# Kernel optimization log

Hardware: AMD Instinct MI355X
Metric: run time of the kernel (lower is better)

## Reference

```python
import jax, jax.numpy as jnp
from jax import lax
import numpy as np

GROUPS = 32

def setup_inputs() -> dict:
    key = jax.random.key(0)
    ks = jax.random.split(key, 12)
    B, C, H, O, N = 4, 256, 256, 256, 4096
    s = 0.02  # small init scale to keep logits in a stable range
    x  = jax.random.normal(ks[0], (B, C, N), dtype=jnp.float32)
    Wk = jax.random.normal(ks[1], (H, C), dtype=jnp.float32) * s
    bk = jax.random.normal(ks[2], (H,), dtype=jnp.float32) * s
    Wq = jax.random.normal(ks[3], (H, C), dtype=jnp.float32) * s
    bq = jax.random.normal(ks[4], (H,), dtype=jnp.float32) * s
    W1 = jax.random.normal(ks[5], (H, C), dtype=jnp.float32) * s
    b1 = jax.random.normal(ks[6], (H,), dtype=jnp.float32) * s
    # grouped conv1d kernel: (out_ch, in_ch // groups, kw) in 'OIH' layout
    W2 = jax.random.normal(ks[7], (H, H // GROUPS, 3), dtype=jnp.float32) * s
    b2 = jax.random.normal(ks[8], (H,), dtype=jnp.float32) * s
    W3 = jax.random.normal(ks[9], (O, H), dtype=jnp.float32) * s
    b3 = jax.random.normal(ks[10], (O,), dtype=jnp.float32) * s
    return {"x": x, "Wk": Wk, "bk": bk, "Wq": Wq, "bq": bq,
            "W1": W1, "b1": b1, "W2": W2, "b2": b2, "W3": W3, "b3": b3}


def reference(x, Wk, bk, Wq, bq, W1, b1, W2, b2, W3, b3):
    # k: 1x1 conv then permute(0,2,1) -> [B, N, H]
    k = jnp.einsum('hc,bcn->bnh', Wk, x) + bk
    # q: 1x1 conv -> [B, H, N]
    q = jnp.einsum('hc,bcn->bhn', Wq, x) + bq[None, :, None]
    # sim = softmax(k @ q, dim=-2): softmax over the FIRST N axis (rows)
    sim = jax.nn.softmax(jnp.einsum('bnh,bhm->bnm', k, q), axis=-2)  # [B, N, N]
    # v path: 1x1 conv -> grouped 3-tap conv (pad=1) -> ReLU -> 1x1 conv
    v1 = jnp.einsum('hc,bcn->bhn', W1, x) + b1[None, :, None]
    v2 = lax.conv_general_dilated(
        v1, W2, window_strides=(1,), padding='SAME',
        feature_group_count=GROUPS,
        dimension_numbers=('NCH', 'OIH', 'NCH')) + b2[None, :, None]
    v2 = jax.nn.relu(v2)
    v = jnp.einsum('oh,bhn->bon', W3, v2) + b3[None, :, None]  # [B, O, N]
    # out = v @ sim -> [B, O, N]
    return jnp.einsum('bon,bnm->bom', v, sim)
```

## Files before the change

kernel.cpp:

```cpp
#include <hip/hip_runtime.h>


#define B_ 4
#define C_ 256
#define H_ 256
#define O_ 256
#define N_ 4096
#define NSPLIT 4
#define SPAN (N_ / NSPLIT)
#define ITERS (SPAN / 32)

typedef short short8 __attribute__((ext_vector_type(8)));
typedef float floatx4 __attribute__((ext_vector_type(4)));
typedef float floatx16 __attribute__((ext_vector_type(16)));

__device__ __forceinline__ unsigned short f2bf(float f) {
  unsigned u = __float_as_uint(f);
  u = (u + 0x7fffu + ((u >> 16) & 1u)) >> 16;
  return (unsigned short)u;
}
__device__ __forceinline__ float bf2f(unsigned short u) {
  return __uint_as_float(((unsigned)u) << 16);
}
__device__ __forceinline__ floatx4 mfma16(short8 a, short8 b, floatx4 c) {
  return __builtin_amdgcn_mfma_f32_16x16x32_bf16(a, b, c, 0, 0, 0);
}
__device__ __forceinline__ floatx16 mfma32(short8 a, short8 b, floatx16 c) {
  return __builtin_amdgcn_mfma_f32_32x32x16_bf16(a, b, c, 0, 0, 0);
}

__global__ __launch_bounds__(256) void prep_kernel(
    const float* __restrict__ Wk, const float* __restrict__ Wq,
    const float* __restrict__ W1, const float* __restrict__ W3,
    unsigned short* __restrict__ wk, unsigned short* __restrict__ wq,
    unsigned short* __restrict__ w1, unsigned short* __restrict__ w3) {
  int i = blockIdx.x * 256 + threadIdx.x;
  wk[i] = f2bf(Wk[i]);
  wq[i] = f2bf(Wq[i]);
  w1[i] = f2bf(W1[i]);
  w3[i] = f2bf(W3[i]);
}

__global__ __launch_bounds__(256) void transpose_kernel(
    const float* __restrict__ x, unsigned short* __restrict__ xt) {
  __shared__ unsigned short tile[64][66];
  const int gid = blockIdx.x;
  const int b  = gid >> 8;
  const int ct = (gid >> 6) & 3;
  const int nt = gid & 63;
  const int c0 = ct * 64, n0 = nt * 64;
  const int t = threadIdx.x;
  const float* xb = x + ((size_t)b * C_ + c0) * N_ + n0;
#pragma unroll
  for (int rr = 0; rr < 4; ++rr) {
    const int c = (t >> 4) + rr * 16;
    const floatx4 v = *reinterpret_cast<const floatx4*>(
        xb + (size_t)c * N_ + (t & 15) * 4);
#pragma unroll
    for (int i = 0; i < 4; ++i) tile[c][(t & 15) * 4 + i] = f2bf(v[i]);
  }
  __syncthreads();
  unsigned short* xo = xt + ((size_t)b * N_ + n0) * C_ + c0;
#pragma unroll
  for (int rr = 0; rr < 2; ++rr) {
    const int nr = (t >> 3) + rr * 32;
    short8 pk;
#pragma unroll
    for (int i = 0; i < 8; ++i) pk[i] = (short)tile[(t & 7) * 8 + i][nr];
    *reinterpret_cast<short8*>(xo + (size_t)nr * C_ + (t & 7) * 8) = pk;
  }
}

__global__ __launch_bounds__(256) void gemm1_kernel(
    const unsigned short* __restrict__ xt,
    const unsigned short* __restrict__ wk, const unsigned short* __restrict__ wq,
    const unsigned short* __restrict__ w1,
    const float* __restrict__ bk, const float* __restrict__ bq,
    const float* __restrict__ b1,
    unsigned short* __restrict__ ko, unsigned short* __restrict__ qo,
    unsigned short* __restrict__ v1o) {
  const int lane = threadIdx.x & 63;
  const int wid  = blockIdx.x * 4 + (threadIdx.x >> 6);
  const int b  = wid >> 9;
  const int r  = wid & 511;
  const int nt = r >> 1;
  const int hh = r & 1;
  const int n0 = nt * 16;
  const int m  = lane & 15;
  const int q  = lane >> 4;

  const unsigned short* xrow = xt + ((size_t)(b * N_) + n0 + m) * C_;
  const unsigned short* Ws[3] = {wk, wq, w1};

  floatx4 acc[3][8];
  const floatx4 z = {0.f, 0.f, 0.f, 0.f};
#pragma unroll
  for (int o = 0; o < 3; ++o)
#pragma unroll
    for (int tt = 0; tt < 8; ++tt) acc[o][tt] = z;

  for (int cs = 0; cs < 8; ++cs) {
    const int cb = cs * 32 + q * 8;
    short8 af = *reinterpret_cast<const short8*>(xrow + cb);
#pragma unroll
    for (int o = 0; o < 3; ++o) {
#pragma unroll
      for (int tt = 0; tt < 8; ++tt) {
        const int h0 = (hh * 8 + tt) * 16;
        short8 bf = *reinterpret_cast<const short8*>(Ws[o] + (h0 + m) * C_ + cb);
        acc[o][tt] = mfma16(af, bf, acc[o][tt]);
      }
    }
  }

#pragma unroll
  for (int tt = 0; tt < 8; ++tt) {
    const int hbase = (hh * 8 + tt) * 2 + (m >> 3);
    const float bias = bk[(hh * 8 + tt) * 16 + m];
#pragma unroll
    for (int r2 = 0; r2 < 4; ++r2) {
      const int n = n0 + q * 4 + r2;
      const int hbl = hbase ^ (n & 7);
      ko[(b * N_ + n) * H_ + hbl * 8 + (m & 7)] = f2bf(acc[0][tt][r2] + bias);
    }
  }
  const float* biases[2] = {bq, b1};
  unsigned short* outs[2] = {qo, v1o};
#pragma unroll
  for (int o = 0; o < 2; ++o) {
#pragma unroll
    for (int tt = 0; tt < 8; ++tt) {
      const int h0 = (hh * 8 + tt) * 16;
      const float bias = biases[o][h0 + m];
#pragma unroll
      for (int r2 = 0; r2 < 4; ++r2) {
        const int n = n0 + q * 4 + r2;
        outs[o][(b * N_ + n) * H_ + h0 + m] = f2bf(acc[o + 1][tt][r2] + bias);
      }
    }
  }
}

__global__ __launch_bounds__(256) void conv_kernel(
    const unsigned short* __restrict__ v1, const float* __restrict__ W2,
    const float* __restrict__ b2, unsigned short* __restrict__ v2) {
  const int h   = threadIdx.x;
  const int blk = blockIdx.x;
  const int b   = blk >> 7;
  const int n0  = (blk & 127) * 32;
  const int g8  = h & ~7;

  float w[24];
#pragma unroll
  for (int i = 0; i < 24; ++i) w[i] = W2[h * 24 + i];
  const float bias = b2[h];
  const unsigned short* vb = v1 + (size_t)b * (N_ * H_) + g8;
  unsigned short* vo = v2 + (size_t)b * (N_ * H_) + h;

  float fp[8], fc[8], fn[8];
  if (n0 == 0) {
#pragma unroll
    for (int i = 0; i < 8; ++i) fp[i] = 0.f;
  } else {
    short8 u = *reinterpret_cast<const short8*>(vb + (size_t)(n0 - 1) * H_);
#pragma unroll
    for (int i = 0; i < 8; ++i) fp[i] = bf2f((unsigned short)u[i]);
  }
  {
    short8 u = *reinterpret_cast<const short8*>(vb + (size_t)n0 * H_);
#pragma unroll
    for (int i = 0; i < 8; ++i) fc[i] = bf2f((unsigned short)u[i]);
  }
#pragma unroll 1
  for (int ns = 0; ns < 32; ++ns) {
    const int n = n0 + ns;
    if (n + 1 < N_) {
      short8 u = *reinterpret_cast<const short8*>(vb + (size_t)(n + 1) * H_);
#pragma unroll
      for (int i = 0; i < 8; ++i) fn[i] = bf2f((unsigned short)u[i]);
    } else {
#pragma unroll
      for (int i = 0; i < 8; ++i) fn[i] = 0.f;
    }
    float acc = bias;
#pragma unroll
    for (int i = 0; i < 8; ++i)
      acc += w[i * 3] * fp[i] + w[i * 3 + 1] * fc[i] + w[i * 3 + 2] * fn[i];
    vo[(size_t)n * H_] = f2bf(fmaxf(acc, 0.f));
#pragma unroll
    for (int i = 0; i < 8; ++i) { fp[i] = fc[i]; fc[i] = fn[i]; }
  }
}

__global__ __launch_bounds__(256) void gemm2_kernel(
    const unsigned short* __restrict__ v2, const unsigned short* __restrict__ w3,
    const float* __restrict__ b3, unsigned short* __restrict__ vo) {
  const int lane = threadIdx.x & 63;
  const int wid  = blockIdx.x * 4 + (threadIdx.x >> 6);
  const int b  = wid >> 9;
  const int r  = wid & 511;
  const int nt = r >> 1;
  const int oh = r & 1;
  const int n0 = nt * 16;
  const int m  = lane & 15;
  const int q  = lane >> 4;

  const unsigned short* vrow = v2 + (b * N_ + n0 + m) * H_;

  floatx4 acc[8];
  const floatx4 z = {0.f, 0.f, 0.f, 0.f};
#pragma unroll
  for (int tt = 0; tt < 8; ++tt) acc[tt] = z;

  for (int hs = 0; hs < 8; ++hs) {
    const int hb = hs * 32 + q * 8;
    short8 bf = *reinterpret_cast<const short8*>(vrow + hb);
#pragma unroll
    for (int tt = 0; tt < 8; ++tt) {
      const int o0 = (oh * 8 + tt) * 16;
      short8 af = *reinterpret_cast<const short8*>(w3 + (o0 + m) * H_ + hb);
      acc[tt] = mfma16(af, bf, acc[tt]);
    }
  }

  const int n  = n0 + m;
  const int n32 = n & ~31;
  const int nb  = (n >> 3) & 3;
  const int nlo = n & 7;
#pragma unroll
  for (int tt = 0; tt < 8; ++tt) {
    const int o0 = (oh * 8 + tt) * 16;
    const floatx4 bb = *reinterpret_cast<const floatx4*>(b3 + o0 + q * 4);
#pragma unroll
    for (int r2 = 0; r2 < 4; ++r2) {
      const int o = o0 + q * 4 + r2;
      const int nbp = nb ^ ((o >> 1) & 3);
      vo[(b * O_ + o) * N_ + n32 + nbp * 8 + nlo] = f2bf(acc[tt][r2] + bb[r2]);
    }
  }
}

__global__ __launch_bounds__(256, 2) void attn_kernel(
    const unsigned short* __restrict__ kbf, const unsigned short* __restrict__ qbf,
    const unsigned short* __restrict__ vbf,
    unsigned short* __restrict__ pacc, float* __restrict__ pml) {
  __shared__ __attribute__((aligned(16))) char smem[2][32768];

  const int ln  = threadIdx.x & 63;
  const int wv  = threadIdx.x >> 6;
  const int gid = blockIdx.x;
  const int t8  = gid & 7;
  const int b   = t8 >> 1;
  const int s   = (t8 & 1) * 2 + ((gid >> 3) & 1);
  const int mw  = (gid >> 4) * 4 + wv;
  const int m0  = mw * 32;
  const int m   = ln & 31;
  const int hl  = ln >> 5;
  const int nbase = s * SPAN;

  const unsigned short* kb2 = kbf + (size_t)b * (N_ * H_);
  const unsigned short* vb2 = vbf + (size_t)b * (O_ * N_);

  const unsigned short* qrow = qbf + ((size_t)(b * N_) + m0 + m) * H_;
  short8 qf[16];
#pragma unroll
  for (int ks = 0; ks < 16; ++ks)
    qf[ks] = *reinterpret_cast<const short8*>(qrow + ks * 16 + hl * 8);

  floatx16 acc[8];
#pragma unroll
  for (int ot = 0; ot < 8; ++ot)
#pragma unroll
    for (int r = 0; r < 16; ++r) acc[ot][r] = 0.f;
  float Lp = 0.f;

  auto stage = [&](int bfi, int nc) {
    const int n0 = nbase + nc * 32;
    const char* kg  = (const char*)kb2 + (size_t)n0 * (H_ * 2);
    const char* vgb = (const char*)vb2 + (size_t)n0 * 2;
    char* lk = &smem[bfi][0];
    char* lv = &smem[bfi][16384];
#pragma unroll
    for (int j = 0; j < 4; ++j) {
      const int ofs = j * 4096 + wv * 1024 + ln * 16;
      __builtin_amdgcn_global_load_lds(
          (const __attribute__((address_space(1))) void*)(kg + ofs),
          (__attribute__((address_space(3))) void*)(lk + ofs), 16, 0, 0);
      const int o = ofs >> 6;
      __builtin_amdgcn_global_load_lds(
          (const __attribute__((address_space(1))) void*)(vgb + (size_t)o * (N_ * 2) + (ofs & 63)),
          (__attribute__((address_space(3))) void*)(lv + ofs), 16, 0, 0);
    }
  };

  stage(0, 0);
  int bufi = 0;

#pragma unroll 1
  for (int nc = 0; nc < ITERS; ++nc) {
    __syncthreads();
    if (nc + 1 < ITERS) stage(bufi ^ 1, nc + 1);

    const char* sk = &smem[bufi][0];
    const char* sv = &smem[bufi][16384];

    floatx16 sacc;
#pragma unroll
    for (int r = 0; r < 16; ++r) sacc[r] = 0.f;
#pragma unroll
    for (int ks = 0; ks < 16; ++ks) {
      short8 kf = *reinterpret_cast<const short8*>(
          sk + m * 512 + (((ks * 2 + hl) ^ (m & 7)) << 4));
      sacc = mfma32(kf, qf[ks], sacc);
    }

    float pv[16];
#pragma unroll
    for (int r = 0; r < 16; ++r) { pv[r] = __expf(sacc[r]); Lp += pv[r]; }

    unsigned wpk[8];
#pragma unroll
    for (int r4 = 0; r4 < 4; ++r4) {
      wpk[r4]     = (unsigned)f2bf(pv[r4])      | ((unsigned)f2bf(pv[r4 + 4])  << 16);
      wpk[r4 + 4] = (unsigned)f2bf(pv[r4 + 8])  | ((unsigned)f2bf(pv[r4 + 12]) << 16);
    }

    short8 pf0, pf1;
#pragma unroll
    for (int j = 0; j < 8; ++j) {
      const int srcLane = m + ((j >> 2) << 5);
      const int u0 = __shfl((int)wpk[j & 3],       srcLane);
      const int u1 = __shfl((int)wpk[(j & 3) + 4], srcLane);
      pf0[j] = (short)(hl ? (u0 >> 16) : (u0 & 0xffff));
      pf1[j] = (short)(hl ? (u1 >> 16) : (u1 & 0xffff));
    }

#pragma unroll
    for (int ot = 0; ot < 8; ++ot) {
      const int o  = ot * 32 + m;
      const int sw = (o >> 1) & 3;
      short8 vf0 = *reinterpret_cast<const short8*>(
          sv + o * 64 + ((hl ^ sw) << 4));
      short8 vf1 = *reinterpret_cast<const short8*>(
          sv + o * 64 + (((2 + hl) ^ sw) << 4));
      acc[ot] = mfma32(vf0, pf0, acc[ot]);
      acc[ot] = mfma32(vf1, pf1, acc[ot]);
    }
    bufi ^= 1;
  }

  float Lv = Lp + __shfl_xor(Lp, 32);
  const float invL = 1.f / Lv;
  const int pwid = (b * 128 + mw) * NSPLIT + s;
  unsigned short* pa = pacc + (size_t)pwid * (O_ * 32);
#pragma unroll
  for (int ot = 0; ot < 8; ++ot)
#pragma unroll
    for (int r = 0; r < 16; ++r) {
      const int row = (r & 3) + ((r >> 2) << 3) + (hl << 2);
      pa[(ot * 32 + row) * 32 + m] = f2bf(acc[ot][r] * invL);
    }
  if (hl == 0) pml[pwid * 32 + m] = Lv;
}

__global__ __launch_bounds__(256) void combine_kernel(
    const unsigned short* __restrict__ pacc, const float* __restrict__ pml,
    float* __restrict__ out) {
  const int blk = blockIdx.x;
  const int b   = blk >> 7;
  const int mw  = blk & 127;
  const int o   = threadIdx.x;
  const int base = (b * 128 + mw) * NSPLIT;

  __shared__ float w[NSPLIT][32];
  if (threadIdx.x < 32) {
    const int c = threadIdx.x;
    float L[NSPLIT], sum = 0.f;
#pragma unroll
    for (int sp = 0; sp < NSPLIT; ++sp) {
      L[sp] = pml[(base + sp) * 32 + c];
      sum += L[sp];
    }
    const float inv = 1.f / sum;
#pragma unroll
    for (int sp = 0; sp < NSPLIT; ++sp) w[sp][c] = L[sp] * inv;
  }
  __syncthreads();

  float res[32];
#pragma unroll
  for (int c = 0; c < 32; ++c) res[c] = 0.f;
#pragma unroll
  for (int sp = 0; sp < NSPLIT; ++sp) {
    const unsigned short* pa =
        pacc + (size_t)(base + sp) * (O_ * 32) + o * 32;
#pragma unroll
    for (int c8 = 0; c8 < 4; ++c8) {
      short8 u = *reinterpret_cast<const short8*>(pa + c8 * 8);
#pragma unroll
      for (int i = 0; i < 8; ++i)
        res[c8 * 8 + i] =
            fmaf(w[sp][c8 * 8 + i], bf2f((unsigned short)u[i]), res[c8 * 8 + i]);
    }
  }
  float* ob = out + ((size_t)(b * O_ + o)) * N_ + mw * 32;
#pragma unroll
  for (int c4 = 0; c4 < 8; ++c4) {
    floatx4 v4 = {res[c4 * 4], res[c4 * 4 + 1], res[c4 * 4 + 2], res[c4 * 4 + 3]};
    *reinterpret_cast<floatx4*>(ob + c4 * 4) = v4;
  }
}

extern "C" void kernel_launch(void* const* d_in, const int* in_sizes, int n_in,
                              void* d_out, int out_size, void* d_ws, size_t ws_size,
                              hipStream_t stream) {
  const float* x  = (const float*)d_in[0];
  const float* Wk = (const float*)d_in[1];
  const float* bk = (const float*)d_in[2];
  const float* Wq = (const float*)d_in[3];
  const float* bq = (const float*)d_in[4];
  const float* W1 = (const float*)d_in[5];
  const float* b1 = (const float*)d_in[6];
  const float* W2 = (const float*)d_in[7];
  const float* b2 = (const float*)d_in[8];
  const float* W3 = (const float*)d_in[9];
  const float* b3 = (const float*)d_in[10];
  float* out = (float*)d_out;

  char* ws = (char*)d_ws;
  const size_t SZ = (size_t)B_ * N_ * H_ * sizeof(unsigned short);
  unsigned short* wkbf = (unsigned short*)(ws);
  unsigned short* wqbf = (unsigned short*)(ws + 131072);
  unsigned short* w1bf = (unsigned short*)(ws + 262144);
  unsigned short* w3bf = (unsigned short*)(ws + 393216);
  char* base = ws + 524288;
  unsigned short* kbf  = (unsigned short*)(base);
  unsigned short* qbf  = (unsigned short*)(base + SZ);
  unsigned short* vbf  = (unsigned short*)(base + 2 * SZ);
  unsigned short* xtbf = (unsigned short*)(base + 3 * SZ);
  unsigned short* v1bf = (unsigned short*)(base + 4 * SZ);
  unsigned short* v2bf = (unsigned short*)(base + 5 * SZ);
  unsigned short* pacc = (unsigned short*)(base + 3 * SZ);
  float*          pml  = (float*)(base + 7 * SZ);

  prep_kernel<<<256, 256, 0, stream>>>(Wk, Wq, W1, W3, wkbf, wqbf, w1bf, w3bf);
  transpose_kernel<<<1024, 256, 0, stream>>>(x, xtbf);
  gemm1_kernel<<<512, 256, 0, stream>>>(xtbf, wkbf, wqbf, w1bf, bk, bq, b1,
                                        kbf, qbf, v1bf);
  conv_kernel<<<512, 256, 0, stream>>>(v1bf, W2, b2, v2bf);
  gemm2_kernel<<<512, 256, 0, stream>>>(v2bf, w3bf, b3, vbf);
  attn_kernel<<<512, 256, 0, stream>>>(kbf, qbf, vbf, pacc, pml);
  combine_kernel<<<512, 256, 0, stream>>>(pacc, pml, out);
}
```

Baseline: 272.8 us.

## Fuse conv with second GEMM, pre-tile K/V layouts, widen attention tile

The grouped conv and the W3 projection now run in one kernel that keeps the ReLU output in LDS, so the v2 round trip through global memory is gone. K and V are written in contiguous 32-row chunks laid out for the attention kernel's MFMA fragments, which makes LDS reads linear and unswizzled. Each attention wave now handles 64 query columns instead of 32, so every K/V LDS fragment feeds two MFMAs; this doubles the accumulator count, drops occupancy to one block per CU and halves the grid. Bf16 packing uses a perm-based truncate-with-rounding helper, and the combine kernel is resized to the 64-wide tiles.

```diff
diff --git a/kernel.cpp b/kernel.cpp
--- a/kernel.cpp
+++ b/kernel.cpp
@@ -27,6 +27,10 @@
 }
 __device__ __forceinline__ floatx16 mfma32(short8 a, short8 b, floatx16 c) {
   return __builtin_amdgcn_mfma_f32_32x32x16_bf16(a, b, c, 0, 0, 0);
+}
+__device__ __forceinline__ unsigned pack2bf(float a, float b) {
+  return __builtin_amdgcn_perm(__float_as_uint(b) + 0x8000u,
+                               __float_as_uint(a) + 0x8000u, 0x07060302u);
 }
 
 __global__ __launch_bounds__(256) void prep_kernel(
@@ -115,13 +119,13 @@
 
 #pragma unroll
   for (int tt = 0; tt < 8; ++tt) {
-    const int hbase = (hh * 8 + tt) * 2 + (m >> 3);
-    const float bias = bk[(hh * 8 + tt) * 16 + m];
+    const int ks16 = hh * 8 + tt;
+    const float bias = bk[ks16 * 16 + m];
 #pragma unroll
     for (int r2 = 0; r2 < 4; ++r2) {
       const int n = n0 + q * 4 + r2;
-      const int hbl = hbase ^ (n & 7);
-      ko[(b * N_ + n) * H_ + hbl * 8 + (m & 7)] = f2bf(acc[0][tt][r2] + bias);
+      ko[((size_t)(b * 128 + (n >> 5))) * 8192 + ks16 * 512 + (n & 31) * 16 + m] =
+          f2bf(acc[0][tt][r2] + bias);
     }
   }
   const float* biases[2] = {bq, b1};
@@ -141,106 +145,98 @@
   }
 }
 
-__global__ __launch_bounds__(256) void conv_kernel(
+__global__ __launch_bounds__(256) void convgemm2_kernel(
     const unsigned short* __restrict__ v1, const float* __restrict__ W2,
-    const float* __restrict__ b2, unsigned short* __restrict__ v2) {
+    const float* __restrict__ b2, const unsigned short* __restrict__ w3,
+    const float* __restrict__ b3, unsigned short* __restrict__ vo) {
+  __shared__ unsigned short v2L[32][264];
+
   const int h   = threadIdx.x;
   const int blk = blockIdx.x;
   const int b   = blk >> 7;
-  const int n0  = (blk & 127) * 32;
+  const int nc  = blk & 127;
+  const int n0  = nc * 32;
   const int g8  = h & ~7;
 
-  float w[24];
-#pragma unroll
-  for (int i = 0; i < 24; ++i) w[i] = W2[h * 24 + i];
-  const float bias = b2[h];
-  const unsigned short* vb = v1 + (size_t)b * (N_ * H_) + g8;
-  unsigned short* vo = v2 + (size_t)b * (N_ * H_) + h;
-
-  float fp[8], fc[8], fn[8];
-  if (n0 == 0) {
-#pragma unroll
-    for (int i = 0; i < 8; ++i) fp[i] = 0.f;
-  } else {
-    short8 u = *reinterpret_cast<const short8*>(vb + (size_t)(n0 - 1) * H_);
-#pragma unroll
-    for (int i = 0; i < 8; ++i) fp[i] = bf2f((unsigned short)u[i]);
-  }
   {
-    short8 u = *reinterpret_cast<const short8*>(vb + (size_t)n0 * H_);
-#pragma unroll
-    for (int i = 0; i < 8; ++i) fc[i] = bf2f((unsigned short)u[i]);
-  }
+    float w[24];
+#pragma unroll
+    for (int i = 0; i < 24; ++i) w[i] = W2[h * 24 + i];
+    const float bias = b2[h];
+    const unsigned short* vb = v1 + (size_t)b * (N_ * H_) + g8;
+
+    float fp[8], fc[8], fn[8];
+    if (n0 == 0) {
+#pragma unroll
+      for (int i = 0; i < 8; ++i) fp[i] = 0.f;
+    } else {
+      short8 u = *reinterpret_cast<const short8*>(vb + (size_t)(n0 - 1) * H_);
+#pragma unroll
+      for (int i = 0; i < 8; ++i) fp[i] = bf2f((unsigned short)u[i]);
+    }
+    {
+      short8 u = *reinterpret_cast<const short8*>(vb + (size_t)n0 * H_);
+#pragma unroll
+      for (int i = 0; i < 8; ++i) fc[i] = bf2f((unsigned short)u[i]);
+    }
 #pragma unroll 1
-  for (int ns = 0; ns < 32; ++ns) {
-    const int n = n0 + ns;
-    if (n + 1 < N_) {
-      short8 u = *reinterpret_cast<const short8*>(vb + (size_t)(n + 1) * H_);
-#pragma unroll
-      for (int i = 0; i < 8; ++i) fn[i] = bf2f((unsigned short)u[i]);
-    } else {
-#pragma unroll
-      for (int i = 0; i < 8; ++i) fn[i] = 0.f;
-    }
-    float acc = bias;
-#pragma unroll
-    for (int i = 0; i < 8; ++i)
-      acc += w[i * 3] * fp[i] + w[i * 3 + 1] * fc[i] + w[i * 3 + 2] * fn[i];
-    vo[(size_t)n * H_] = f2bf(fmaxf(acc, 0.f));
-#pragma unroll
-    for (int i = 0; i < 8; ++i) { fp[i] = fc[i]; fc[i] = fn[i]; }
-  }
-}
-
-__global__ __launch_bounds__(256) void gemm2_kernel(
-    const unsigned short* __restrict__ v2, const unsigned short* __restrict__ w3,
-    const float* __restrict__ b3, unsigned short* __restrict__ vo) {
-  const int lane = threadIdx.x & 63;
-  const int wid  = blockIdx.x * 4 + (threadIdx.x >> 6);
-  const int b  = wid >> 9;
-  const int r  = wid & 511;
-  const int nt = r >> 1;
-  const int oh = r & 1;
-  const int n0 = nt * 16;
-  const int m  = lane & 15;
-  const int q  = lane >> 4;
-
-  const unsigned short* vrow = v2 + (b * N_ + n0 + m) * H_;
-
-  floatx4 acc[8];
-  const floatx4 z = {0.f, 0.f, 0.f, 0.f};
-#pragma unroll
-  for (int tt = 0; tt < 8; ++tt) acc[tt] = z;
-
-  for (int hs = 0; hs < 8; ++hs) {
-    const int hb = hs * 32 + q * 8;
-    short8 bf = *reinterpret_cast<const short8*>(vrow + hb);
-#pragma unroll
-    for (int tt = 0; tt < 8; ++tt) {
-      const int o0 = (oh * 8 + tt) * 16;
-      short8 af = *reinterpret_cast<const short8*>(w3 + (o0 + m) * H_ + hb);
-      acc[tt] = mfma16(af, bf, acc[tt]);
-    }
-  }
-
-  const int n  = n0 + m;
-  const int n32 = n & ~31;
-  const int nb  = (n >> 3) & 3;
-  const int nlo = n & 7;
-#pragma unroll
-  for (int tt = 0; tt < 8; ++tt) {
-    const int o0 = (oh * 8 + tt) * 16;
-    const floatx4 bb = *reinterpret_cast<const floatx4*>(b3 + o0 + q * 4);
-#pragma unroll
-    for (int r2 = 0; r2 < 4; ++r2) {
-      const int o = o0 + q * 4 + r2;
-      const int nbp = nb ^ ((o >> 1) & 3);
-      vo[(b * O_ + o) * N_ + n32 + nbp * 8 + nlo] = f2bf(acc[tt][r2] + bb[r2]);
-    }
-  }
-}
-
-__global__ __launch_bounds__(256, 2) void attn_kernel(
+    for (int ns = 0; ns < 32; ++ns) {
+      const int n = n0 + ns;
+      if (n + 1 < N_) {
+        short8 u = *reinterpret_cast<const short8*>(vb + (size_t)(n + 1) * H_);
+#pragma unroll
+        for (int i = 0; i < 8; ++i) fn[i] = bf2f((unsigned short)u[i]);
+      } else {
+#pragma unroll
+        for (int i = 0; i < 8; ++i) fn[i] = 0.f;
+      }
+      float a = bias;
+#pragma unroll
+      for (int i = 0; i < 8; ++i)
+        a += w[i * 3] * fp[i] + w[i * 3 + 1] * fc[i] + w[i * 3 + 2] * fn[i];
+      v2L[ns][h] = f2bf(fmaxf(a, 0.f));
+#pragma unroll
+      for (int i = 0; i < 8; ++i) { fp[i] = fc[i]; fc[i] = fn[i]; }
+    }
+  }
+  __syncthreads();
+
+  const int ln = threadIdx.x & 63;
+  const int wv = threadIdx.x >> 6;
+  const int m  = ln & 31;
+  const int hl = ln >> 5;
+
+  floatx16 acc2[2];
+#pragma unroll
+  for (int ot = 0; ot < 2; ++ot)
+#pragma unroll
+    for (int r = 0; r < 16; ++r) acc2[ot][r] = 0.f;
+
+#pragma unroll
+  for (int ks = 0; ks < 16; ++ks) {
+    short8 bfr = *reinterpret_cast<const short8*>(&v2L[m][ks * 16 + hl * 8]);
+#pragma unroll
+    for (int ot = 0; ot < 2; ++ot) {
+      const int o0 = wv * 64 + ot * 32;
+      short8 afr = *reinterpret_cast<const short8*>(
+          w3 + (o0 + m) * H_ + ks * 16 + hl * 8);
+      acc2[ot] = mfma32(afr, bfr, acc2[ot]);
+    }
+  }
+
+  const int kn  = (m >> 4) & 1;
+  const int nlo = m & 15;
+  unsigned short* vc = vo + ((size_t)(b * 128 + nc) * 2 + kn) * 4096 + nlo;
+#pragma unroll
+  for (int ot = 0; ot < 2; ++ot)
+#pragma unroll
+    for (int r = 0; r < 16; ++r) {
+      const int o = wv * 64 + ot * 32 + (r & 3) + 8 * (r >> 2) + 4 * hl;
+      vc[o * 16] = f2bf(acc2[ot][r] + b3[o]);
+    }
+}
+
+__global__ __launch_bounds__(256, 1) void attn_kernel(
     const unsigned short* __restrict__ kbf, const unsigned short* __restrict__ qbf,
     const unsigned short* __restrict__ vbf,
     unsigned short* __restrict__ pacc, float* __restrict__ pml) {
@@ -249,35 +245,36 @@
   const int ln  = threadIdx.x & 63;
   const int wv  = threadIdx.x >> 6;
   const int gid = blockIdx.x;
-  const int t8  = gid & 7;
-  const int b   = t8 >> 1;
-  const int s   = (t8 & 1) * 2 + ((gid >> 3) & 1);
-  const int mw  = (gid >> 4) * 4 + wv;
-  const int m0  = mw * 32;
+  const int b   = gid & 3;
+  const int s   = (gid >> 2) & 3;
+  const int mt256 = gid >> 4;
+  const int mt64  = mt256 * 4 + wv;
+  const int m0  = mt64 * 64;
   const int m   = ln & 31;
   const int hl  = ln >> 5;
-  const int nbase = s * SPAN;
-
-  const unsigned short* kb2 = kbf + (size_t)b * (N_ * H_);
-  const unsigned short* vb2 = vbf + (size_t)b * (O_ * N_);
-
-  const unsigned short* qrow = qbf + ((size_t)(b * N_) + m0 + m) * H_;
-  short8 qf[16];
-#pragma unroll
-  for (int ks = 0; ks < 16; ++ks)
-    qf[ks] = *reinterpret_cast<const short8*>(qrow + ks * 16 + hl * 8);
-
-  floatx16 acc[8];
-#pragma unroll
-  for (int ot = 0; ot < 8; ++ot)
-#pragma unroll
-    for (int r = 0; r < 16; ++r) acc[ot][r] = 0.f;
-  float Lp = 0.f;
+  const int lane_base = m * 32 + hl * 16;
+
+  short8 qf[2][16];
+#pragma unroll
+  for (int mh = 0; mh < 2; ++mh) {
+    const unsigned short* qrow =
+        qbf + ((size_t)b * N_ + m0 + mh * 32 + m) * H_ + hl * 8;
+#pragma unroll
+    for (int ks = 0; ks < 16; ++ks)
+      qf[mh][ks] = *reinterpret_cast<const short8*>(qrow + ks * 16);
+  }
+
+  floatx16 acc[16];
+#pragma unroll
+  for (int t = 0; t < 16; ++t)
+#pragma unroll
+    for (int r = 0; r < 16; ++r) acc[t][r] = 0.f;
+  float Lp0 = 0.f, Lp1 = 0.f;
 
   auto stage = [&](int bfi, int nc) {
-    const int n0 = nbase + nc * 32;
-    const char* kg  = (const char*)kb2 + (size_t)n0 * (H_ * 2);
-    const char* vgb = (const char*)vb2 + (size_t)n0 * 2;
+    const size_t row = (size_t)(b * 128 + s * 32 + nc);
+    const char* kg = (const char*)(kbf + row * 8192);
+    const char* vg = (const char*)(vbf + row * 8192);
     char* lk = &smem[bfi][0];
     char* lv = &smem[bfi][16384];
 #pragma unroll
@@ -286,15 +283,15 @@
       __builtin_amdgcn_global_load_lds(
           (const __attribute__((address_space(1))) void*)(kg + ofs),
           (__attribute__((address_space(3))) void*)(lk + ofs), 16, 0, 0);
-      const int o = ofs >> 6;
       __builtin_amdgcn_global_load_lds(
-          (const __attribute__((address_space(1))) void*)(vgb + (size_t)o * (N_ * 2) + (ofs & 63)),
+          (const __attribute__((address_space(1))) void*)(vg + ofs),
           (__attribute__((address_space(3))) void*)(lv + ofs), 16, 0, 0);
     }
   };
 
   stage(0, 0);
   int bufi = 0;
+  const int hlsh = hl * 16;
 
 #pragma unroll 1
   for (int nc = 0; nc < ITERS; ++nc) {
@@ -304,81 +301,95 @@
     const char* sk = &smem[bufi][0];
     const char* sv = &smem[bufi][16384];
 
-    floatx16 sacc;
-#pragma unroll
-    for (int r = 0; r < 16; ++r) sacc[r] = 0.f;
+    floatx16 s0, s1;
+#pragma unroll
+    for (int r = 0; r < 16; ++r) { s0[r] = 0.f; s1[r] = 0.f; }
 #pragma unroll
     for (int ks = 0; ks < 16; ++ks) {
-      short8 kf = *reinterpret_cast<const short8*>(
-          sk + m * 512 + (((ks * 2 + hl) ^ (m & 7)) << 4));
-      sacc = mfma32(kf, qf[ks], sacc);
-    }
-
-    float pv[16];
-#pragma unroll
-    for (int r = 0; r < 16; ++r) { pv[r] = __expf(sacc[r]); Lp += pv[r]; }
-
-    unsigned wpk[8];
+      short8 kf = *reinterpret_cast<const short8*>(sk + lane_base + ks * 1024);
+      s0 = mfma32(kf, qf[0][ks], s0);
+      s1 = mfma32(kf, qf[1][ks], s1);
+    }
+
+    unsigned wpk0[8], wpk1[8];
 #pragma unroll
     for (int r4 = 0; r4 < 4; ++r4) {
-      wpk[r4]     = (unsigned)f2bf(pv[r4])      | ((unsigned)f2bf(pv[r4 + 4])  << 16);
-      wpk[r4 + 4] = (unsigned)f2bf(pv[r4 + 8])  | ((unsigned)f2bf(pv[r4 + 12]) << 16);
-    }
-
-    short8 pf0, pf1;
+      float a0 = __expf(s0[r4]),      b0 = __expf(s0[r4 + 4]);
+      float c0 = __expf(s0[r4 + 8]),  d0 = __expf(s0[r4 + 12]);
+      float a1 = __expf(s1[r4]),      b1 = __expf(s1[r4 + 4]);
+      float c1 = __expf(s1[r4 + 8]),  d1 = __expf(s1[r4 + 12]);
+      Lp0 += (a0 + b0) + (c0 + d0);
+      Lp1 += (a1 + b1) + (c1 + d1);
+      wpk0[r4]     = pack2bf(a0, b0);
+      wpk0[r4 + 4] = pack2bf(c0, d0);
+      wpk1[r4]     = pack2bf(a1, b1);
+      wpk1[r4 + 4] = pack2bf(c1, d1);
+    }
+
+    short8 pf[2][2];
 #pragma unroll
     for (int j = 0; j < 8; ++j) {
       const int srcLane = m + ((j >> 2) << 5);
-      const int u0 = __shfl((int)wpk[j & 3],       srcLane);
-      const int u1 = __shfl((int)wpk[(j & 3) + 4], srcLane);
-      pf0[j] = (short)(hl ? (u0 >> 16) : (u0 & 0xffff));
-      pf1[j] = (short)(hl ? (u1 >> 16) : (u1 & 0xffff));
+      const int u00 = __shfl((int)wpk0[j & 3],       srcLane);
+      const int u01 = __shfl((int)wpk0[(j & 3) + 4], srcLane);
+      const int u10 = __shfl((int)wpk1[j & 3],       srcLane);
+      const int u11 = __shfl((int)wpk1[(j & 3) + 4], srcLane);
+      pf[0][0][j] = (short)((unsigned)u00 >> hlsh);
+      pf[0][1][j] = (short)((unsigned)u01 >> hlsh);
+      pf[1][0][j] = (short)((unsigned)u10 >> hlsh);
+      pf[1][1][j] = (short)((unsigned)u11 >> hlsh);
     }
 
 #pragma unroll
     for (int ot = 0; ot < 8; ++ot) {
-      const int o  = ot * 32 + m;
-      const int sw = (o >> 1) & 3;
-      short8 vf0 = *reinterpret_cast<const short8*>(
-          sv + o * 64 + ((hl ^ sw) << 4));
-      short8 vf1 = *reinterpret_cast<const short8*>(
-          sv + o * 64 + (((2 + hl) ^ sw) << 4));
-      acc[ot] = mfma32(vf0, pf0, acc[ot]);
-      acc[ot] = mfma32(vf1, pf1, acc[ot]);
+#pragma unroll
+      for (int kn = 0; kn < 2; ++kn) {
+        short8 vf = *reinterpret_cast<const short8*>(
+            sv + lane_base + kn * 8192 + ot * 1024);
+        acc[ot]     = mfma32(vf, pf[0][kn], acc[ot]);
+        acc[8 + ot] = mfma32(vf, pf[1][kn], acc[8 + ot]);
+      }
     }
     bufi ^= 1;
   }
 
-  float Lv = Lp + __shfl_xor(Lp, 32);
-  const float invL = 1.f / Lv;
-  const int pwid = (b * 128 + mw) * NSPLIT + s;
-  unsigned short* pa = pacc + (size_t)pwid * (O_ * 32);
-#pragma unroll
-  for (int ot = 0; ot < 8; ++ot)
-#pragma unroll
-    for (int r = 0; r < 16; ++r) {
-      const int row = (r & 3) + ((r >> 2) << 3) + (hl << 2);
-      pa[(ot * 32 + row) * 32 + m] = f2bf(acc[ot][r] * invL);
-    }
-  if (hl == 0) pml[pwid * 32 + m] = Lv;
+  float Lv0 = Lp0 + __shfl_xor(Lp0, 32);
+  float Lv1 = Lp1 + __shfl_xor(Lp1, 32);
+  const float i0 = 1.f / Lv0, i1 = 1.f / Lv1;
+
+  const int pwid = (b * 64 + mt64) * NSPLIT + s;
+  unsigned short* pa = pacc + (size_t)pwid * (O_ * 64);
+#pragma unroll
+  for (int mh = 0; mh < 2; ++mh) {
+    const float inv = mh ? i1 : i0;
+#pragma unroll
+    for (int ot = 0; ot < 8; ++ot)
+#pragma unroll
+      for (int r = 0; r < 16; ++r) {
+        const int o = ot * 32 + (r & 3) + 8 * (r >> 2) + 4 * hl;
+        pa[o * 64 + mh * 32 + m] = f2bf(acc[mh * 8 + ot][r] * inv);
+      }
+  }
+  if (hl == 0) pml[pwid * 64 + m] = Lv0;
+  else         pml[pwid * 64 + 32 + m] = Lv1;
 }
 
 __global__ __launch_bounds__(256) void combine_kernel(
     const unsigned short* __restrict__ pacc, const float* __restrict__ pml,
     float* __restrict__ out) {
   const int blk = blockIdx.x;
-  const int b   = blk >> 7;
-  const int mw  = blk & 127;
+  const int b   = blk >> 6;
+  const int mt  = blk & 63;
   const int o   = threadIdx.x;
-  const int base = (b * 128 + mw) * NSPLIT;
-
-  __shared__ float w[NSPLIT][32];
-  if (threadIdx.x < 32) {
+  const int base = (b * 64 + mt) * NSPLIT;
+
+  __shared__ float w[NSPLIT][64];
+  if (threadIdx.x < 64) {
     const int c = threadIdx.x;
     float L[NSPLIT], sum = 0.f;
 #pragma unroll
     for (int sp = 0; sp < NSPLIT; ++sp) {
-      L[sp] = pml[(base + sp) * 32 + c];
+      L[sp] = pml[(base + sp) * 64 + c];
       sum += L[sp];
     }
     const float inv = 1.f / sum;
@@ -387,15 +398,15 @@
   }
   __syncthreads();
 
-  float res[32];
-#pragma unroll
-  for (int c = 0; c < 32; ++c) res[c] = 0.f;
+  float res[64];
+#pragma unroll
+  for (int c = 0; c < 64; ++c) res[c] = 0.f;
 #pragma unroll
   for (int sp = 0; sp < NSPLIT; ++sp) {
     const unsigned short* pa =
-        pacc + (size_t)(base + sp) * (O_ * 32) + o * 32;
-#pragma unroll
-    for (int c8 = 0; c8 < 4; ++c8) {
+        pacc + (size_t)(base + sp) * (O_ * 64) + o * 64;
+#pragma unroll
+    for (int c8 = 0; c8 < 8; ++c8) {
       short8 u = *reinterpret_cast<const short8*>(pa + c8 * 8);
 #pragma unroll
       for (int i = 0; i < 8; ++i)
@@ -403,9 +414,9 @@
             fmaf(w[sp][c8 * 8 + i], bf2f((unsigned short)u[i]), res[c8 * 8 + i]);
     }
   }
-  float* ob = out + ((size_t)(b * O_ + o)) * N_ + mw * 32;
-#pragma unroll
-  for (int c4 = 0; c4 < 8; ++c4) {
+  float* ob = out + ((size_t)(b * O_ + o)) * N_ + mt * 64;
+#pragma unroll
+  for (int c4 = 0; c4 < 16; ++c4) {
     floatx4 v4 = {res[c4 * 4], res[c4 * 4 + 1], res[c4 * 4 + 2], res[c4 * 4 + 3]};
     *reinterpret_cast<floatx4*>(ob + c4 * 4) = v4;
   }
@@ -439,7 +450,6 @@
   unsigned short* vbf  = (unsigned short*)(base + 2 * SZ);
   unsigned short* xtbf = (unsigned short*)(base + 3 * SZ);
   unsigned short* v1bf = (unsigned short*)(base + 4 * SZ);
-  unsigned short* v2bf = (unsigned short*)(base + 5 * SZ);
   unsigned short* pacc = (unsigned short*)(base + 3 * SZ);
   float*          pml  = (float*)(base + 7 * SZ);
 
@@ -447,8 +457,7 @@
   transpose_kernel<<<1024, 256, 0, stream>>>(x, xtbf);
   gemm1_kernel<<<512, 256, 0, stream>>>(xtbf, wkbf, wqbf, w1bf, bk, bq, b1,
                                         kbf, qbf, v1bf);
-  conv_kernel<<<512, 256, 0, stream>>>(v1bf, W2, b2, v2bf);
-  gemm2_kernel<<<512, 256, 0, stream>>>(v2bf, w3bf, b3, vbf);
-  attn_kernel<<<512, 256, 0, stream>>>(kbf, qbf, vbf, pacc, pml);
-  combine_kernel<<<512, 256, 0, stream>>>(pacc, pml, out);
-}
+  convgemm2_kernel<<<512, 256, 0, stream>>>(v1bf, W2, b2, w3bf, b3, vbf);
+  attn_kernel<<<256, 256, 0, stream>>>(kbf, qbf, vbf, pacc, pml);
+  combine_kernel<<<256, 256, 0, stream>>>(pacc, pml, out);
+}
```

After: 722.8 us. 165% more time.
